# Kernel optimization log

Hardware: AMD Instinct MI355X
Metric: run time of the kernel (lower is better)

The kernel has to match this reference:

```python
import jax, jax.numpy as jnp
from jax import lax
import numpy as np

B, IN, OUT = 32768, 512, 512


def _bit_length(a):
    # a: nonnegative int32. Smear high bit down, then popcount == bit length.
    y = a
    y = y | (y >> 1)
    y = y | (y >> 2)
    y = y | (y >> 4)
    y = y | (y >> 8)
    y = y | (y >> 16)
    return lax.population_count(y)


def trunc_top_bits(v, k=4):
    # compress_top4(|a|,|b|,4): keep top-k significant bits of each magnitude.
    a = jnp.abs(v)
    shift = jnp.maximum(_bit_length(a) - k, 0)
    t = (a >> shift) << shift
    return t * jnp.sign(v)


def setup_inputs() -> dict:
    key = jax.random.key(0)
    k1, k2, k3 = jax.random.split(key, 3)
    bound = 1.0 / np.sqrt(IN)  # matches kaiming_uniform(a=sqrt(5)) + bias bound
    x = jax.random.normal(k1, (B, IN), dtype=jnp.float32)
    weight = jax.random.uniform(k2, (OUT, IN), dtype=jnp.float32, minval=-bound, maxval=bound)
    bias = jax.random.uniform(k3, (OUT,), dtype=jnp.float32, minval=-bound, maxval=bound)
    return {"x": x, "weight": weight, "bias": bias, "weight_sf": 8, "act_sf": 6}


def reference(x, weight, bias, weight_sf, act_sf):
    # Fixed-point quantization: input / 2^{-sf} then trunc-toward-zero int cast
    xi = (x * (2.0 ** act_sf)).astype(jnp.int32)       # [B, IN]
    wi = (weight * (2.0 ** weight_sf)).astype(jnp.int32)  # [OUT, IN]
    # sign/abs decomposition + top-4-bit truncated multiply-accumulate:
    # sum_y compress_top4(|xi|,|wi|) * sign(xi)*sign(wi) == dot of signed truncs
    tx = trunc_top_bits(xi).astype(jnp.float32)
    tw = trunc_top_bits(wi).astype(jnp.float32)
    acc = jnp.einsum("bi,oi->bo", tx, tw)             # [B, OUT], exact in fp32
    scale = (2.0 ** (-act_sf)) * (2.0 ** (-weight_sf))
    return acc * scale + bias[None, :]
```

## Files before the change

kernel.cpp:

```cpp
#include <hip/hip_runtime.h>
#include <hip/hip_bf16.h>
#include <stdint.h>

#define B_DIM 32768
#define IN_DIM 512
#define OUT_DIM 512

typedef __bf16 bf16;
typedef bf16 bf16x8 __attribute__((ext_vector_type(8)));
typedef float f32x4 __attribute__((ext_vector_type(4)));

__device__ __forceinline__ uint32_t quant2(float a, float b, float scale) {
    uint32_t ua = __float_as_uint(truncf(a * scale));
    uint32_t ub = __float_as_uint(truncf(b * scale));
    uint32_t p = __builtin_amdgcn_perm(ub, ua, 0x07060302u);
    return p & 0xFFF0FFF0u;
}

__global__ void quant_kernel(const float* __restrict__ in, bf16* __restrict__ out,
                             int n4, const int* __restrict__ sf) {
    int i = blockIdx.x * blockDim.x + threadIdx.x;
    if (i >= n4) return;
    float scale = (float)(1 << *sf);
    float4 v = ((const float4*)in)[i];
    uint2 p;
    p.x = quant2(v.x, v.y, scale);
    p.y = quant2(v.z, v.w, scale);
    ((uint2*)out)[i] = p;
}

__global__ __launch_bounds__(256, 3)
void gemm_fused(const float* __restrict__ X, const bf16* __restrict__ W,
                const float* __restrict__ bias, float* __restrict__ C,
                const int* __restrict__ wsf, const int* __restrict__ asf) {
    __shared__ bf16 As[128 * 64];
    __shared__ bf16 Bs[128 * 64];

    const int t    = threadIdx.x;
    const int w    = t >> 6;
    const int lane = t & 63;

    const int b    = blockIdx.x;
    const int xcd  = b & 7;
    const int slot = b >> 3;
    const int bm   = xcd * 32 + (slot >> 2);
    const int bn   = slot & 3;
    const int row0 = bm * 128;
    const int col0 = bn * 128;
    const int wm   = (w & 1) * 64;
    const int wn   = (w >> 1) * 64;

    const int m_st = t >> 3;
    const int kub  = (t & 7) ^ (m_st & 7);
    const size_t offB = (size_t)(col0 + m_st) * IN_DIM + kub * 8;

    const int r_a = t >> 1;
    const int h_a = t & 1;
    const float* xrow = X + (size_t)(row0 + r_a) * IN_DIM + h_a * 32;

    const float ascale = (float)(1 << *asf);

    f32x4 acc[4][4];
    #pragma unroll
    for (int mt = 0; mt < 4; ++mt)
        #pragma unroll
        for (int nt = 0; nt < 4; ++nt)
            acc[mt][nt] = 0.0f;

    float4 fr[8];
    #pragma unroll
    for (int j = 0; j < 8; ++j)
        fr[j] = *((const float4*)xrow + j);
    uint4 pk[4];
    #pragma unroll
    for (int j = 0; j < 4; ++j) {
        pk[j].x = quant2(fr[2 * j].x, fr[2 * j].y, ascale);
        pk[j].y = quant2(fr[2 * j].z, fr[2 * j].w, ascale);
        pk[j].z = quant2(fr[2 * j + 1].x, fr[2 * j + 1].y, ascale);
        pk[j].w = quant2(fr[2 * j + 1].z, fr[2 * j + 1].w, ascale);
    }

    for (int k0 = 0; k0 < IN_DIM; k0 += 64) {
        #pragma unroll
        for (int j = 0; j < 4; ++j) {
            bf16* adst = As + (size_t)(r_a * 8 + ((h_a * 4 + j) ^ (r_a & 7))) * 8;
            *(uint4*)adst = pk[j];
        }
        #pragma unroll
        for (int i = 0; i < 4; ++i) {
            const bf16* gb = W + offB + (size_t)i * 32 * IN_DIM + k0;
            bf16*       lb = Bs + (i * 256 + w * 64) * 8;
            __builtin_amdgcn_global_load_lds((const __attribute__((address_space(1))) void*)gb,
                                             (__attribute__((address_space(3))) void*)lb, 16, 0, 0);
        }
        const bool more = (k0 + 64) < IN_DIM;
        if (more) {
            #pragma unroll
            for (int j = 0; j < 8; ++j)
                fr[j] = *((const float4*)(xrow + k0 + 64) + j);
        }
        __syncthreads();
        if (more) {
            #pragma unroll
            for (int j = 0; j < 4; ++j) {
                pk[j].x = quant2(fr[2 * j].x, fr[2 * j].y, ascale);
                pk[j].y = quant2(fr[2 * j].z, fr[2 * j].w, ascale);
                pk[j].z = quant2(fr[2 * j + 1].x, fr[2 * j + 1].y, ascale);
                pk[j].w = quant2(fr[2 * j + 1].z, fr[2 * j + 1].w, ascale);
            }
        }

        const int q  = lane >> 4;
        const int rl = lane & 15;
        const int sx = rl & 7;
        #pragma unroll
        for (int ks = 0; ks < 2; ++ks) {
            const int c  = ks * 4 + q;
            const int cs = (c ^ sx) * 8;
            bf16x8 af[4], bfr[4];
            #pragma unroll
            for (int mt = 0; mt < 4; ++mt)
                af[mt] = *(const bf16x8*)(As + (wm + mt * 16 + rl) * 64 + cs);
            #pragma unroll
            for (int nt = 0; nt < 4; ++nt)
                bfr[nt] = *(const bf16x8*)(Bs + (wn + nt * 16 + rl) * 64 + cs);
            #pragma unroll
            for (int mt = 0; mt < 4; ++mt)
                #pragma unroll
                for (int nt = 0; nt < 4; ++nt)
                    acc[mt][nt] = __builtin_amdgcn_mfma_f32_16x16x32_bf16(af[mt], bfr[nt], acc[mt][nt], 0, 0, 0);
        }
        __syncthreads();
    }

    const float oscale = ldexpf(1.0f, -(*wsf + *asf));
    const int cl = lane & 15;
    const int rg = (lane >> 4) * 4;
    #pragma unroll
    for (int nt = 0; nt < 4; ++nt) {
        const int col = col0 + wn + nt * 16 + cl;
        const float bv = bias[col];
        #pragma unroll
        for (int mt = 0; mt < 4; ++mt) {
            f32x4 a = acc[mt][nt];
            #pragma unroll
            for (int r = 0; r < 4; ++r) {
                const int row = row0 + wm + mt * 16 + rg + r;
                C[(size_t)row * OUT_DIM + col] = a[r] * oscale + bv;
            }
        }
    }
}

extern "C" void kernel_launch(void* const* d_in, const int* in_sizes, int n_in,
                              void* d_out, int out_size, void* d_ws, size_t ws_size,
                              hipStream_t stream) {
    const float* x    = (const float*)d_in[0];
    const float* wgt  = (const float*)d_in[1];
    const float* bias = (const float*)d_in[2];
    const int*   wsf  = (const int*)d_in[3];
    const int*   asf  = (const int*)d_in[4];

    bf16* tw = (bf16*)d_ws;

    const int nw4 = OUT_DIM * IN_DIM / 4;
    quant_kernel<<<(nw4 + 255) / 256, 256, 0, stream>>>(wgt, tw, nw4, wsf);

    const int grid = (B_DIM / 128) * (OUT_DIM / 128);
    gemm_fused<<<grid, 256, 0, stream>>>(x, tw, bias, (float*)d_out, wsf, asf);
}
```

Baseline: 155.4 us.

## Double-buffer LDS tiles to overlap next-tile loads with MFMA compute

Turns the single-buffered K loop into a ping-pong scheme with two LDS buffers for A and B. The loads for the next tile are issued before the current tile's MFMAs, then quantized and stored to the other buffer, so each iteration needs one barrier instead of two. LDS use doubles to 64 KB per block and the launch bound drops from 3 to 2 waves per SIMD, which may reduce occupancy and latency hiding across blocks. The loop is fully unrolled, and explicit waitcnt and scheduling barriers are added.

```diff
diff --git a/kernel.cpp b/kernel.cpp
--- a/kernel.cpp
+++ b/kernel.cpp
@@ -29,12 +29,12 @@
     ((uint2*)out)[i] = p;
 }
 
-__global__ __launch_bounds__(256, 3)
+__global__ __launch_bounds__(256, 2)
 void gemm_fused(const float* __restrict__ X, const bf16* __restrict__ W,
                 const float* __restrict__ bias, float* __restrict__ C,
                 const int* __restrict__ wsf, const int* __restrict__ asf) {
-    __shared__ bf16 As[128 * 64];
-    __shared__ bf16 Bs[128 * 64];
+    __shared__ bf16 As[2][128 * 64];
+    __shared__ bf16 Bs[2][128 * 64];
 
     const int t    = threadIdx.x;
     const int w    = t >> 6;
@@ -67,70 +67,95 @@
         for (int nt = 0; nt < 4; ++nt)
             acc[mt][nt] = 0.0f;
 
-    float4 fr[8];
+    float4 fr[2][8];
+    uint4 pk[4];
+
+    #pragma unroll
+    for (int i = 0; i < 4; ++i) {
+        const bf16* gb = W + offB + (size_t)i * 32 * IN_DIM;
+        bf16*       lb = &Bs[0][(i * 256 + w * 64) * 8];
+        __builtin_amdgcn_global_load_lds((const __attribute__((address_space(1))) void*)gb,
+                                         (__attribute__((address_space(3))) void*)lb, 16, 0, 0);
+    }
     #pragma unroll
     for (int j = 0; j < 8; ++j)
-        fr[j] = *((const float4*)xrow + j);
-    uint4 pk[4];
+        fr[0][j] = ((const float4*)xrow)[j];
     #pragma unroll
     for (int j = 0; j < 4; ++j) {
-        pk[j].x = quant2(fr[2 * j].x, fr[2 * j].y, ascale);
-        pk[j].y = quant2(fr[2 * j].z, fr[2 * j].w, ascale);
-        pk[j].z = quant2(fr[2 * j + 1].x, fr[2 * j + 1].y, ascale);
-        pk[j].w = quant2(fr[2 * j + 1].z, fr[2 * j + 1].w, ascale);
+        pk[j].x = quant2(fr[0][2 * j].x, fr[0][2 * j].y, ascale);
+        pk[j].y = quant2(fr[0][2 * j].z, fr[0][2 * j].w, ascale);
+        pk[j].z = quant2(fr[0][2 * j + 1].x, fr[0][2 * j + 1].y, ascale);
+        pk[j].w = quant2(fr[0][2 * j + 1].z, fr[0][2 * j + 1].w, ascale);
     }
+    #pragma unroll
+    for (int j = 0; j < 4; ++j) {
+        bf16* adst = &As[0][(size_t)(r_a * 8 + ((h_a * 4 + j) ^ (r_a & 7))) * 8];
+        *(uint4*)adst = pk[j];
+    }
+    asm volatile("s_waitcnt vmcnt(0) lgkmcnt(0)" ::: "memory");
+    __builtin_amdgcn_sched_barrier(0);
+    __builtin_amdgcn_s_barrier();
+    __builtin_amdgcn_sched_barrier(0);
 
-    for (int k0 = 0; k0 < IN_DIM; k0 += 64) {
-        #pragma unroll
-        for (int j = 0; j < 4; ++j) {
-            bf16* adst = As + (size_t)(r_a * 8 + ((h_a * 4 + j) ^ (r_a & 7))) * 8;
-            *(uint4*)adst = pk[j];
-        }
-        #pragma unroll
-        for (int i = 0; i < 4; ++i) {
-            const bf16* gb = W + offB + (size_t)i * 32 * IN_DIM + k0;
-            bf16*       lb = Bs + (i * 256 + w * 64) * 8;
-            __builtin_amdgcn_global_load_lds((const __attribute__((address_space(1))) void*)gb,
-                                             (__attribute__((address_space(3))) void*)lb, 16, 0, 0);
-        }
-        const bool more = (k0 + 64) < IN_DIM;
-        if (more) {
+    #pragma unroll
+    for (int k = 0; k < 8; ++k) {
+        const int cur = k & 1;
+        const int nxt = cur ^ 1;
+
+        if (k < 7) {
+            #pragma unroll
+            for (int i = 0; i < 4; ++i) {
+                const bf16* gb = W + offB + (size_t)i * 32 * IN_DIM + (k + 1) * 64;
+                bf16*       lb = &Bs[nxt][(i * 256 + w * 64) * 8];
+                __builtin_amdgcn_global_load_lds((const __attribute__((address_space(1))) void*)gb,
+                                                 (__attribute__((address_space(3))) void*)lb, 16, 0, 0);
+            }
             #pragma unroll
             for (int j = 0; j < 8; ++j)
-                fr[j] = *((const float4*)(xrow + k0 + 64) + j);
+                fr[nxt][j] = ((const float4*)(xrow + (k + 1) * 64))[j];
         }
-        __syncthreads();
-        if (more) {
+
+        {
+            const int q  = lane >> 4;
+            const int rl = lane & 15;
+            const int sx = rl & 7;
             #pragma unroll
-            for (int j = 0; j < 4; ++j) {
-                pk[j].x = quant2(fr[2 * j].x, fr[2 * j].y, ascale);
-                pk[j].y = quant2(fr[2 * j].z, fr[2 * j].w, ascale);
-                pk[j].z = quant2(fr[2 * j + 1].x, fr[2 * j + 1].y, ascale);
-                pk[j].w = quant2(fr[2 * j + 1].z, fr[2 * j + 1].w, ascale);
+            for (int ks = 0; ks < 2; ++ks) {
+                const int c  = ks * 4 + q;
+                const int cs = (c ^ sx) * 8;
+                bf16x8 af[4], bfr[4];
+                #pragma unroll
+                for (int mt = 0; mt < 4; ++mt)
+                    af[mt] = *(const bf16x8*)(&As[cur][0] + (wm + mt * 16 + rl) * 64 + cs);
+                #pragma unroll
+                for (int nt = 0; nt < 4; ++nt)
+                    bfr[nt] = *(const bf16x8*)(&Bs[cur][0] + (wn + nt * 16 + rl) * 64 + cs);
+                #pragma unroll
+                for (int mt = 0; mt < 4; ++mt)
+                    #pragma unroll
+                    for (int nt = 0; nt < 4; ++nt)
+                        acc[mt][nt] = __builtin_amdgcn_mfma_f32_16x16x32_bf16(af[mt], bfr[nt], acc[mt][nt], 0, 0, 0);
             }
         }
 
-        const int q  = lane >> 4;
-        const int rl = lane & 15;
-        const int sx = rl & 7;
-        #pragma unroll
-        for (int ks = 0; ks < 2; ++ks) {
-            const int c  = ks * 4 + q;
-            const int cs = (c ^ sx) * 8;
-            bf16x8 af[4], bfr[4];
+        if (k < 7) {
             #pragma unroll
-            for (int mt = 0; mt < 4; ++mt)
-                af[mt] = *(const bf16x8*)(As + (wm + mt * 16 + rl) * 64 + cs);
+            for (int j = 0; j < 4; ++j) {
+                pk[j].x = quant2(fr[nxt][2 * j].x, fr[nxt][2 * j].y, ascale);
+                pk[j].y = quant2(fr[nxt][2 * j].z, fr[nxt][2 * j].w, ascale);
+                pk[j].z = quant2(fr[nxt][2 * j + 1].x, fr[nxt][2 * j + 1].y, ascale);
+                pk[j].w = quant2(fr[nxt][2 * j + 1].z, fr[nxt][2 * j + 1].w, ascale);
+            }
             #pragma unroll
-            for (int nt = 0; nt < 4; ++nt)
-                bfr[nt] = *(const bf16x8*)(Bs + (wn + nt * 16 + rl) * 64 + cs);
-            #pragma unroll
-            for (int mt = 0; mt < 4; ++mt)
-                #pragma unroll
-                for (int nt = 0; nt < 4; ++nt)
-                    acc[mt][nt] = __builtin_amdgcn_mfma_f32_16x16x32_bf16(af[mt], bfr[nt], acc[mt][nt], 0, 0, 0);
+            for (int j = 0; j < 4; ++j) {
+                bf16* adst = &As[nxt][(size_t)(r_a * 8 + ((h_a * 4 + j) ^ (r_a & 7))) * 8];
+                *(uint4*)adst = pk[j];
+            }
+            asm volatile("s_waitcnt vmcnt(0) lgkmcnt(0)" ::: "memory");
+            __builtin_amdgcn_sched_barrier(0);
+            __builtin_amdgcn_s_barrier();
+            __builtin_amdgcn_sched_barrier(0);
         }
-        __syncthreads();
     }
 
     const float oscale = ldexpf(1.0f, -(*wsf + *asf));
```

Result: no change. 155.3 us (-0.0%).
